# Kernel optimization log

Measured on AMD Instinct MI355X. Metric: run time of the kernel, lower is better.

## Reference

```python
import jax, jax.numpy as jnp
import numpy as np

IN_DIM = 256
OUT_DIM = 256

def setup_inputs() -> dict:
    key = jax.random.key(0)
    k1, k2, k3, k4 = jax.random.split(key, 4)
    B, N, K, D = 4, 10000, 16, IN_DIM
    x = jax.random.normal(k1, (B, N, D), dtype=jnp.float32)
    neigh = jax.random.randint(k2, (N, K), 0, N, dtype=jnp.int64)
    # nn.Linear(2*in_dim, out_dim): W [out, 2*in], b [out]
    bound = 1.0 / np.sqrt(2 * D)
    W = jax.random.uniform(k3, (OUT_DIM, 2 * D), minval=-bound, maxval=bound, dtype=jnp.float32)
    b = jax.random.uniform(k4, (OUT_DIM,), minval=-bound, maxval=bound, dtype=jnp.float32)
    return {"x": x, "neigh": neigh, "W": W, "b": b}

def reference(x, neigh, W, b):
    # x: [B,N,D], neigh: [N,K] with -1 = padding
    mask = (neigh >= 0)                                # [N,K]
    idx = jnp.clip(neigh, 0, None)                     # [N,K]
    # batch_gather_nodes: x_nei[b,n,k,:] = x[b, idx[n,k], :]
    x_nei = x[:, idx, :]                               # [B,N,K,D]
    x_nei = x_nei * mask[None, :, :, None].astype(x.dtype)
    denom = jnp.clip(mask.sum(axis=1), 1, None).astype(x.dtype)  # [N]
    agg = x_nei.sum(axis=2) / denom[None, :, None]     # [B,N,D]
    h = jnp.concatenate([x, agg], axis=-1)             # [B,N,2D]
    return jax.nn.relu(jnp.einsum('bnd,od->bno', h, W) + b)
```

## Files before the change

### kernel.cpp

```cpp
#include <hip/hip_runtime.h>
#include <hip/hip_bf16.h>
#include <stdint.h>

#define B_   4
#define N_   10000
#define K_   16
#define D_   256
#define OUT_ 256
#define M_   (B_ * N_)
#define CW   32
#define NCH  8
#define CHUNK_ELEMS ((size_t)N_ * B_ * CW)
#define TILES_ 625
#define TPH    16384

typedef __attribute__((ext_vector_type(8))) short          short8;
typedef __attribute__((ext_vector_type(8))) unsigned short ushort8;
typedef __attribute__((ext_vector_type(4))) float          f32x4;
typedef __attribute__((ext_vector_type(4))) unsigned short ushort4_t;

__device__ inline unsigned short f2bf(float f) {
    __hip_bfloat16 h = __float2bfloat16(f);
    return *reinterpret_cast<unsigned short*>(&h);
}
__device__ inline float bf2f(unsigned short u) {
    unsigned int v = ((unsigned int)u) << 16;
    return __builtin_bit_cast(float, v);
}

__global__ __launch_bounds__(256) void wprep(const float* __restrict__ W,
                                             unsigned short* __restrict__ Wb) {
    const int g  = blockIdx.x * 256 + threadIdx.x;
    const int h  = g >> 14;
    const int t  = g & 16383;
    const int ks = t >> 12;
    const int rr = (t >> 4) & 255;
    const int kg = (t & 15) * 4;
    const float4 v = *(const float4*)(W + (size_t)rr * 512 + h * 256 + ks * 64 + kg);
    ushort4_t s;
    s.x = f2bf(v.x); s.y = f2bf(v.y); s.z = f2bf(v.z); s.w = f2bf(v.w);
    const int off = ((rr * 128 + kg * 2) ^ ((rr & 7) << 4)) >> 1;
    *(ushort4_t*)(Wb + (size_t)(h * 4 + ks) * TPH + off) = s;
}

__global__ __launch_bounds__(512) void gemm3(const float* __restrict__ x,
                                             const unsigned short* __restrict__ Wb,
                                             float* __restrict__ y1,
                                             unsigned short* __restrict__ y2c) {
    __shared__ unsigned short As[64 * 64];
    __shared__ unsigned short Bs[256 * 64];

    const int tid  = threadIdx.x;
    const int w    = tid >> 6;
    const int lane = tid & 63;
    const int q    = lane >> 4;
    const int r16  = lane & 15;
    const int wm   = w >> 2;
    const int wn   = w & 3;

    const int bi   = blockIdx.x;
    const int xcd  = bi & 7;
    const int u    = bi >> 3;
    const int g    = (u >> 1) * 8 + xcd;
    const int half = u & 1;
    if (g >= TILES_) return;
    const int tile_m = g * 64;

    const int arow = tid >> 3;
    const int akg  = (tid & 7) * 8;
    const float* ap = x + (size_t)(tile_m + arow) * D_ + akg;
    const unsigned int awoff = (unsigned)((arow * 128 + akg * 2) ^ ((arow & 7) << 4));

    const unsigned short* wsrc0 = Wb + (size_t)(half * 4) * TPH + tid * 8;

    const unsigned int sw = (unsigned)((r16 & 7) << 4);

    f32x4 acc[2][4] = {};

    float4 c0 = *(const float4*)ap;
    float4 c1 = *(const float4*)(ap + 4);
#pragma unroll
    for (int i2 = 0; i2 < 4; ++i2) {
        __builtin_amdgcn_global_load_lds(
            (const __attribute__((address_space(1))) void*)(wsrc0 + i2 * 4096),
            (__attribute__((address_space(3))) void*)(Bs + tid * 8 + i2 * 4096),
            16, 0, 0);
    }
    {
        ushort8 s;
        s[0] = f2bf(c0.x); s[1] = f2bf(c0.y); s[2] = f2bf(c0.z); s[3] = f2bf(c0.w);
        s[4] = f2bf(c1.x); s[5] = f2bf(c1.y); s[6] = f2bf(c1.z); s[7] = f2bf(c1.w);
        *(ushort8*)((char*)As + awoff) = s;
    }
    __syncthreads();

#pragma unroll
    for (int ks = 0; ks < 4; ++ks) {
        float4 n0, n1;
        if (ks < 3) {
            n0 = *(const float4*)(ap + (ks + 1) * 64);
            n1 = *(const float4*)(ap + (ks + 1) * 64 + 4);
        }

#pragma unroll
        for (int ksub = 0; ksub < 2; ++ksub) {
            short8 a[2], bf[4];
#pragma unroll
            for (int i = 0; i < 2; ++i) {
                const unsigned int ad =
                    (unsigned)((wm * 32 + i * 16 + r16) * 128 + ksub * 64 + q * 16) ^ sw;
                a[i] = *(const short8*)((const char*)As + ad);
            }
#pragma unroll
            for (int j = 0; j < 4; ++j) {
                const unsigned int bd =
                    (unsigned)((wn * 64 + j * 16 + r16) * 128 + ksub * 64 + q * 16) ^ sw;
                bf[j] = *(const short8*)((const char*)Bs + bd);
            }
            if (half == 0) {
#pragma unroll
                for (int i = 0; i < 2; ++i)
#pragma unroll
                    for (int j = 0; j < 4; ++j)
                        acc[i][j] = __builtin_amdgcn_mfma_f32_16x16x32_bf16(a[i], bf[j], acc[i][j], 0, 0, 0);
            } else {
#pragma unroll
                for (int i = 0; i < 2; ++i)
#pragma unroll
                    for (int j = 0; j < 4; ++j)
                        acc[i][j] = __builtin_amdgcn_mfma_f32_16x16x32_bf16(bf[j], a[i], acc[i][j], 0, 0, 0);
            }
        }

        if (ks < 3) {
            __syncthreads();
            const unsigned short* wsrc = wsrc0 + (size_t)(ks + 1) * TPH;
#pragma unroll
            for (int i2 = 0; i2 < 4; ++i2) {
                __builtin_amdgcn_global_load_lds(
                    (const __attribute__((address_space(1))) void*)(wsrc + i2 * 4096),
                    (__attribute__((address_space(3))) void*)(Bs + tid * 8 + i2 * 4096),
                    16, 0, 0);
            }
            ushort8 s;
            s[0] = f2bf(n0.x); s[1] = f2bf(n0.y); s[2] = f2bf(n0.z); s[3] = f2bf(n0.w);
            s[4] = f2bf(n1.x); s[5] = f2bf(n1.y); s[6] = f2bf(n1.z); s[7] = f2bf(n1.w);
            *(ushort8*)((char*)As + awoff) = s;
            __syncthreads();
        }
    }

    if (half == 0) {
#pragma unroll
        for (int i = 0; i < 2; ++i) {
#pragma unroll
            for (int reg = 0; reg < 4; ++reg) {
                const int m = tile_m + wm * 32 + i * 16 + q * 4 + reg;
                float* row = y1 + (size_t)m * OUT_ + wn * 64;
#pragma unroll
                for (int j = 0; j < 4; ++j)
                    row[j * 16 + r16] = acc[i][j][reg];
            }
        }
    } else {
#pragma unroll
        for (int i = 0; i < 2; ++i) {
            const int m  = tile_m + wm * 32 + i * 16 + r16;
            const int bb = (m >= N_) + (m >= 2 * N_) + (m >= 3 * N_);
            const int n  = m - bb * N_;
            unsigned short* rb = y2c + (size_t)(n * B_ + bb) * CW;
#pragma unroll
            for (int j = 0; j < 4; ++j) {
                const int o2  = wn * 64 + j * 16 + q * 4;
                const int cch = o2 >> 5;
                const int col = o2 & 31;
                ushort4_t p;
                p.x = f2bf(acc[i][j][0]); p.y = f2bf(acc[i][j][1]);
                p.z = f2bf(acc[i][j][2]); p.w = f2bf(acc[i][j][3]);
                *(ushort4_t*)(rb + (size_t)cch * CHUNK_ELEMS + col) = p;
            }
        }
    }
}

__global__ __launch_bounds__(256) void gather_out(const unsigned short* __restrict__ y2c,
                                                  const float* __restrict__ y1,
                                                  const int*   __restrict__ neigh,
                                                  const float* __restrict__ bias,
                                                  float* __restrict__ out) {
    const int c   = blockIdx.x & 7;
    const int g   = blockIdx.x >> 3;
    const int n0  = g * 16;
    const int tid = threadIdx.x;

    __shared__ int   idx_s[16 * K_];
    __shared__ float inv_s[16];

    idx_s[tid] = neigh[n0 * K_ + tid];
    __syncthreads();
    if (tid < 16) {
        int cnt = 0;
#pragma unroll
        for (int k = 0; k < K_; ++k) cnt += idx_s[tid * K_ + k] >= 0 ? 1 : 0;
        inv_s[tid] = 1.0f / (float)(cnt > 1 ? cnt : 1);
    }
    __syncthreads();

    const int q  = tid & 3;
    const int tl = tid >> 2;
    const int ns = tl >> 2;
    const int b  = tl & 3;

    const unsigned short* ycc = y2c + (size_t)c * CHUNK_ELEMS;

    int jj[K_];
#pragma unroll
    for (int k = 0; k < K_; ++k) jj[k] = idx_s[ns * K_ + k];

    ushort8 vv[K_];
#pragma unroll
    for (int k = 0; k < K_; ++k) {
        const int jc = jj[k] >= 0 ? jj[k] : 0;
        vv[k] = *(const ushort8*)(ycc + ((size_t)jc * B_ + b) * CW + q * 8);
    }

    const size_t mo = (size_t)(b * N_ + n0 + ns) * OUT_ + c * CW + q * 8;
    const f32x4 s0 = *(const f32x4*)(y1 + mo);
    const f32x4 s1 = *(const f32x4*)(y1 + mo + 4);
    const f32x4 b0 = *(const f32x4*)(bias + c * CW + q * 8);
    const f32x4 b1 = *(const f32x4*)(bias + c * CW + q * 8 + 4);

    float acc[8] = {0.f, 0.f, 0.f, 0.f, 0.f, 0.f, 0.f, 0.f};
#pragma unroll
    for (int k = 0; k < K_; ++k) {
        const float m = jj[k] >= 0 ? 1.f : 0.f;
#pragma unroll
        for (int e = 0; e < 8; ++e) acc[e] += bf2f(vv[k][e]) * m;
    }
    const float inv = inv_s[ns];

    f32x4 o0, o1;
#pragma unroll
    for (int e = 0; e < 4; ++e) {
        float v0 = acc[e] * inv + s0[e] + b0[e];
        float v1 = acc[e + 4] * inv + s1[e] + b1[e];
        o0[e] = v0 > 0.f ? v0 : 0.f;
        o1[e] = v1 > 0.f ? v1 : 0.f;
    }
    __builtin_nontemporal_store(o0, (f32x4*)(out + mo));
    __builtin_nontemporal_store(o1, (f32x4*)(out + mo + 4));
}

extern "C" void kernel_launch(void* const* d_in, const int* in_sizes, int n_in,
                              void* d_out, int out_size, void* d_ws, size_t ws_size,
                              hipStream_t stream) {
    const float* x     = (const float*)d_in[0];
    const int*   neigh = (const int*)d_in[1];
    const float* W     = (const float*)d_in[2];
    const float* bias  = (const float*)d_in[3];
    float*       out   = (float*)d_out;

    unsigned short* Wb  = (unsigned short*)d_ws;
    float*          y1  = (float*)(Wb + 8 * TPH);
    unsigned short* y2c = (unsigned short*)(y1 + (size_t)M_ * OUT_);

    wprep<<<128, 256, 0, stream>>>(W, Wb);
    gemm3<<<158 * 8, 256 * 2, 0, stream>>>(x, Wb, y1, y2c);
    gather_out<<<(N_ / 16) * NCH, 256, 0, stream>>>(y2c, y1, neigh, bias, out);
}
```

Before: 140.7 us.

## Re-chunk GEMM outputs into narrow column slabs and shrink gather blocks

The GEMM's self-term output y1 now goes out in a chunked, node-major layout (8 floats per row per chunk) using the same transposed MFMA orientation as the neighbour term. The neighbour projection y2c moves from 32-wide to 16-wide bf16 chunks. The gather kernel now launches 10000 blocks of 128 threads, each handling a 16-column slab, so each gathered row is 32 bytes. The aim is contiguous vector stores from the GEMM and smaller, more cache-friendly gather footprints per chunk, at the cost of more blocks and narrower random reads.

```diff
diff --git a/kernel.cpp b/kernel.cpp
--- a/kernel.cpp
+++ b/kernel.cpp
@@ -8,11 +8,11 @@
 #define D_   256
 #define OUT_ 256
 #define M_   (B_ * N_)
-#define CW   32
-#define NCH  8
-#define CHUNK_ELEMS ((size_t)N_ * B_ * CW)
 #define TILES_ 625
 #define TPH    16384
+
+#define C16_ELEMS ((size_t)M_ * 16)
+#define C8_ELEMS  ((size_t)M_ * 8)
 
 typedef __attribute__((ext_vector_type(8))) short          short8;
 typedef __attribute__((ext_vector_type(8))) unsigned short ushort8;
@@ -45,7 +45,7 @@
 
 __global__ __launch_bounds__(512) void gemm3(const float* __restrict__ x,
                                              const unsigned short* __restrict__ Wb,
-                                             float* __restrict__ y1,
+                                             float* __restrict__ y1c,
                                              unsigned short* __restrict__ y2c) {
     __shared__ unsigned short As[64 * 64];
     __shared__ unsigned short Bs[256 * 64];
@@ -117,19 +117,11 @@
                     (unsigned)((wn * 64 + j * 16 + r16) * 128 + ksub * 64 + q * 16) ^ sw;
                 bf[j] = *(const short8*)((const char*)Bs + bd);
             }
-            if (half == 0) {
-#pragma unroll
-                for (int i = 0; i < 2; ++i)
-#pragma unroll
-                    for (int j = 0; j < 4; ++j)
-                        acc[i][j] = __builtin_amdgcn_mfma_f32_16x16x32_bf16(a[i], bf[j], acc[i][j], 0, 0, 0);
-            } else {
-#pragma unroll
-                for (int i = 0; i < 2; ++i)
-#pragma unroll
-                    for (int j = 0; j < 4; ++j)
-                        acc[i][j] = __builtin_amdgcn_mfma_f32_16x16x32_bf16(bf[j], a[i], acc[i][j], 0, 0, 0);
-            }
+#pragma unroll
+            for (int i = 0; i < 2; ++i)
+#pragma unroll
+                for (int j = 0; j < 4; ++j)
+                    acc[i][j] = __builtin_amdgcn_mfma_f32_16x16x32_bf16(bf[j], a[i], acc[i][j], 0, 0, 0);
         }
 
         if (ks < 3) {
@@ -150,53 +142,51 @@
         }
     }
 
-    if (half == 0) {
-#pragma unroll
-        for (int i = 0; i < 2; ++i) {
-#pragma unroll
-            for (int reg = 0; reg < 4; ++reg) {
-                const int m = tile_m + wm * 32 + i * 16 + q * 4 + reg;
-                float* row = y1 + (size_t)m * OUT_ + wn * 64;
-#pragma unroll
-                for (int j = 0; j < 4; ++j)
-                    row[j * 16 + r16] = acc[i][j][reg];
-            }
-        }
-    } else {
-#pragma unroll
-        for (int i = 0; i < 2; ++i) {
-            const int m  = tile_m + wm * 32 + i * 16 + r16;
-            const int bb = (m >= N_) + (m >= 2 * N_) + (m >= 3 * N_);
-            const int n  = m - bb * N_;
-            unsigned short* rb = y2c + (size_t)(n * B_ + bb) * CW;
+#pragma unroll
+    for (int i = 0; i < 2; ++i) {
+        const int m  = tile_m + wm * 32 + i * 16 + r16;
+        const int bb = (m >= N_) + (m >= 2 * N_) + (m >= 3 * N_);
+        const int n  = m - bb * N_;
+        const size_t row = (size_t)(n * B_ + bb);
+        if (half == 0) {
 #pragma unroll
             for (int j = 0; j < 4; ++j) {
-                const int o2  = wn * 64 + j * 16 + q * 4;
-                const int cch = o2 >> 5;
-                const int col = o2 & 31;
+                const int o2 = wn * 64 + j * 16 + q * 4;
+                f32x4 p;
+                p[0] = acc[i][j][0]; p[1] = acc[i][j][1];
+                p[2] = acc[i][j][2]; p[3] = acc[i][j][3];
+                *(f32x4*)(y1c + (size_t)(o2 >> 3) * C8_ELEMS + row * 8 + (o2 & 7)) = p;
+            }
+        } else {
+#pragma unroll
+            for (int j = 0; j < 4; ++j) {
+                const int o2 = wn * 64 + j * 16 + q * 4;
                 ushort4_t p;
                 p.x = f2bf(acc[i][j][0]); p.y = f2bf(acc[i][j][1]);
                 p.z = f2bf(acc[i][j][2]); p.w = f2bf(acc[i][j][3]);
-                *(ushort4_t*)(rb + (size_t)cch * CHUNK_ELEMS + col) = p;
-            }
-        }
-    }
-}
-
-__global__ __launch_bounds__(256) void gather_out(const unsigned short* __restrict__ y2c,
-                                                  const float* __restrict__ y1,
+                *(ushort4_t*)(y2c + (size_t)(o2 >> 4) * C16_ELEMS + row * 16 + (o2 & 15)) = p;
+            }
+        }
+    }
+}
+
+__global__ __launch_bounds__(128) void gather_out(const unsigned short* __restrict__ y2c,
+                                                  const float* __restrict__ y1c,
                                                   const int*   __restrict__ neigh,
                                                   const float* __restrict__ bias,
                                                   float* __restrict__ out) {
-    const int c   = blockIdx.x & 7;
-    const int g   = blockIdx.x >> 3;
+    const int bi  = blockIdx.x;
+    const int lo  = bi < 5000;
+    const int c   = (bi & 7) + (lo ? 0 : 8);
+    const int g   = (lo ? bi : bi - 5000) >> 3;
     const int n0  = g * 16;
     const int tid = threadIdx.x;
 
     __shared__ int   idx_s[16 * K_];
     __shared__ float inv_s[16];
 
-    idx_s[tid] = neigh[n0 * K_ + tid];
+    idx_s[tid]       = neigh[n0 * K_ + tid];
+    idx_s[tid + 128] = neigh[n0 * K_ + tid + 128];
     __syncthreads();
     if (tid < 16) {
         int cnt = 0;
@@ -206,12 +196,12 @@
     }
     __syncthreads();
 
-    const int q  = tid & 3;
-    const int tl = tid >> 2;
+    const int h  = tid & 1;
+    const int tl = tid >> 1;
     const int ns = tl >> 2;
     const int b  = tl & 3;
 
-    const unsigned short* ycc = y2c + (size_t)c * CHUNK_ELEMS;
+    const unsigned short* ycc = y2c + (size_t)c * C16_ELEMS;
 
     int jj[K_];
 #pragma unroll
@@ -221,14 +211,15 @@
 #pragma unroll
     for (int k = 0; k < K_; ++k) {
         const int jc = jj[k] >= 0 ? jj[k] : 0;
-        vv[k] = *(const ushort8*)(ycc + ((size_t)jc * B_ + b) * CW + q * 8);
-    }
-
-    const size_t mo = (size_t)(b * N_ + n0 + ns) * OUT_ + c * CW + q * 8;
-    const f32x4 s0 = *(const f32x4*)(y1 + mo);
-    const f32x4 s1 = *(const f32x4*)(y1 + mo + 4);
-    const f32x4 b0 = *(const f32x4*)(bias + c * CW + q * 8);
-    const f32x4 b1 = *(const f32x4*)(bias + c * CW + q * 8 + 4);
+        vv[k] = *(const ushort8*)(ycc + ((size_t)jc * B_ + b) * 16 + h * 8);
+    }
+
+    const size_t row = (size_t)((n0 + ns) * B_ + b);
+    const float* yrow = y1c + (size_t)(2 * c + h) * C8_ELEMS + row * 8;
+    const f32x4 s0 = *(const f32x4*)(yrow);
+    const f32x4 s1 = *(const f32x4*)(yrow + 4);
+    const f32x4 b0 = *(const f32x4*)(bias + c * 16 + h * 8);
+    const f32x4 b1 = *(const f32x4*)(bias + c * 16 + h * 8 + 4);
 
     float acc[8] = {0.f, 0.f, 0.f, 0.f, 0.f, 0.f, 0.f, 0.f};
 #pragma unroll
@@ -247,8 +238,9 @@
         o0[e] = v0 > 0.f ? v0 : 0.f;
         o1[e] = v1 > 0.f ? v1 : 0.f;
     }
-    __builtin_nontemporal_store(o0, (f32x4*)(out + mo));
-    __builtin_nontemporal_store(o1, (f32x4*)(out + mo + 4));
+    float* op = out + ((size_t)b * N_ + n0 + ns) * OUT_ + c * 16 + h * 8;
+    __builtin_nontemporal_store(o0, (f32x4*)op);
+    __builtin_nontemporal_store(o1, (f32x4*)(op + 4));
 }
 
 extern "C" void kernel_launch(void* const* d_in, const int* in_sizes, int n_in,
@@ -261,10 +253,10 @@
     float*       out   = (float*)d_out;
 
     unsigned short* Wb  = (unsigned short*)d_ws;
-    float*          y1  = (float*)(Wb + 8 * TPH);
-    unsigned short* y2c = (unsigned short*)(y1 + (size_t)M_ * OUT_);
-
+    float*          y1c = (float*)(Wb + 8 * TPH);
+    unsigned short* y2c = (unsigned short*)(y1c + 32 * C8_ELEMS);
+    
     wprep<<<128, 256, 0, stream>>>(W, Wb);
-    gemm3<<<158 * 8, 256 * 2, 0, stream>>>(x, Wb, y1, y2c);
-    gather_out<<<(N_ / 16) * NCH, 256, 0, stream>>>(y2c, y1, neigh, bias, out);
-}
+    gemm3<<<158 * 8, 512, 0, stream>>>(x, Wb, y1c, y2c);
+    gather_out<<<10000, 128, 0, stream>>>(y2c, y1c, neigh, bias, out);
+}
```

Result: slower. 157.2 us (+11.7%).
